# Optimization experiments

Measured on AMD Instinct MI355X. Metric: run time of the kernel, lower is better.

The kernel has to match this reference:

```python
import jax, jax.numpy as jnp
import numpy as np

B, L, D = 16, 8192, 256

def setup_inputs() -> dict:
    key = jax.random.key(0)
    inputs = jax.random.normal(key, (B, L, D), dtype=jnp.float32)
    return {"inputs": inputs}

def reference(inputs) -> jnp.ndarray:
    # position weights: softmax over L of per-token L2 norms
    norms = jnp.linalg.norm(inputs, axis=2)            # [B, L]
    w = jax.nn.softmax(norms, axis=1)                  # [B, L]
    # weighted sum of outer products == X^T diag(w) X, fused as one einsum
    out = jnp.einsum('bl,bld,ble->bde', w, inputs, inputs)  # [B, D, D]
    return out
```

## Files before the change

kernel.cpp:

```cpp
#include <hip/hip_runtime.h>
#include <hip/hip_bf16.h>

#define NB 16
#define NL 8192
#define ND 256
#define KSPLIT 16
#define CHUNK (NL / KSPLIT)
#define BK 64

#define WS_G_OFF 256

typedef __bf16 bf16_t;
typedef __attribute__((ext_vector_type(4))) __bf16 bf16x4;
typedef __attribute__((ext_vector_type(8))) __bf16 bf16x8;
typedef __attribute__((ext_vector_type(4))) float floatx4;

__device__ __forceinline__ int fsw(int col) {
    return ((col >> 2) & 7) ^ ((col & 3) << 1);
}

__global__ __launch_bounds__(1024, 4) void k_gemm(const float* __restrict__ x,
                                                  float* __restrict__ ws,
                                                  float* __restrict__ gram) {
    const int ks = blockIdx.x, b = blockIdx.y;
    const int t = threadIdx.x;
    const int lane = t & 63;
    const int w = __builtin_amdgcn_readfirstlane(t >> 6);
    const int quad = lane >> 4, m = lane & 15;
    const int g = w >> 1, h = w & 1;

    __shared__ bf16_t lds[256 * 64];

    const float* xb = x + (size_t)b * NL * ND;
    const int l0 = ks * CHUNK;

    floatx4 acc[9];
    #pragma unroll
    for (int j = 0; j < 9; ++j)
        #pragma unroll
        for (int r = 0; r < 4; ++r) acc[j][r] = 0.f;

    float e_acc = 0.f;
    float4 xv[4];
    {
        const float* gp = xb + (size_t)(l0 + w * 4) * ND + lane * 4;
        #pragma unroll
        for (int j = 0; j < 4; ++j) xv[j] = *(const float4*)(gp + (size_t)j * ND);
    }

    for (int kk = 0; kk < CHUNK; kk += BK) {
        if (kk) __syncthreads();
        {
            float ss[4];
            #pragma unroll
            for (int j = 0; j < 4; ++j)
                ss[j] = xv[j].x * xv[j].x + xv[j].y * xv[j].y
                      + xv[j].z * xv[j].z + xv[j].w * xv[j].w;
            #pragma unroll
            for (int off = 32; off; off >>= 1) {
                #pragma unroll
                for (int j = 0; j < 4; ++j) ss[j] += __shfl_xor(ss[j], off, 64);
            }
            float s[4];
            #pragma unroll
            for (int j = 0; j < 4; ++j) {
                s[j] = __expf(0.5f * sqrtf(ss[j]));
                e_acc += s[j] * s[j];
            }
            bf16x4 p[4];
            #pragma unroll
            for (int j = 0; j < 4; ++j) {
                const float* vf = (const float*)&xv[j];
                #pragma unroll
                for (int c = 0; c < 4; ++c) p[c][j] = (bf16_t)(vf[c] * s[j]);
            }
            #pragma unroll
            for (int c = 0; c < 4; ++c) {
                const int col = 4 * lane + c;
                *(bf16x4*)(&lds[col * 64 + ((g ^ fsw(col)) << 3) + (h << 2)]) = p[c];
            }
        }
        __syncthreads();
        if (kk + BK < CHUNK) {
            const float* gp = xb + (size_t)(l0 + kk + BK + w * 4) * ND + lane * 4;
            #pragma unroll
            for (int j = 0; j < 4; ++j) xv[j] = *(const float4*)(gp + (size_t)j * ND);
        }
        #pragma unroll
        for (int k2 = 0; k2 < 2; ++k2) {
            const int kcq = k2 * 4 + quad;
            const int col0 = (w << 4) + m;
            const bf16x8 f0 = *(const bf16x8*)(&lds[(col0 << 6) + ((kcq ^ fsw(col0)) << 3)]);
            #pragma unroll
            for (int j = 0; j < 9; ++j) {
                const int col = (((w + j) & 15) << 4) + m;
                const bf16x8 fj = *(const bf16x8*)(&lds[(col << 6) + ((kcq ^ fsw(col)) << 3)]);
                acc[j] = __builtin_amdgcn_mfma_f32_16x16x32_bf16(f0, fj, acc[j], 0, 0, 0);
            }
        }
    }

    __shared__ float red[16];
    if (lane == 0) red[w] = e_acc;
    __syncthreads();
    if (t == 0) {
        float z = 0.f;
        #pragma unroll
        for (int i = 0; i < 16; ++i) z += red[i];
        ws[b * 16 + ks] = z;
    }

    float* gb = gram + (size_t)(ks * NB + b) * 144 * 256;
    #pragma unroll
    for (int j = 0; j < 9; ++j) {
        float* tb = gb + (w * 9 + j) * 256 + quad * 64 + m;
        #pragma unroll
        for (int reg = 0; reg < 4; ++reg) tb[reg * 16] = acc[j][reg];
    }
}

__global__ __launch_bounds__(256) void k_reduce(const float* __restrict__ gram,
                                                const float* __restrict__ ws,
                                                float* __restrict__ out) {
    const int t = threadIdx.x;
    const int sg = t >> 6;
    const int f = t & 63;
    const int gslot = blockIdx.x * 4 + sg;
    const int b = gslot / 144;
    const int slot = gslot - b * 144;
    const int rt = slot / 9;
    const int j = slot - rt * 9;
    const int ct = (rt + j) & 15;
    const int er = f >> 2, ecq = f & 3;

    const float* gp = gram + ((size_t)b * 144 + slot) * 256 + er * 16 + ecq * 4;
    float4 s = make_float4(0.f, 0.f, 0.f, 0.f);
    #pragma unroll
    for (int ks = 0; ks < KSPLIT; ++ks) {
        const float4 v = *(const float4*)(gp + (size_t)ks * (NB * 144 * 256));
        s.x += v.x; s.y += v.y; s.z += v.z; s.w += v.w;
    }

    float z = 0.f;
    #pragma unroll
    for (int ks = 0; ks < KSPLIT; ++ks) z += ws[b * 16 + ks];
    const float zi = 1.0f / z;
    s.x *= zi; s.y *= zi; s.z *= zi; s.w *= zi;

    float* ob = out + (size_t)b * ND * ND;
    *(float4*)(ob + (size_t)(rt * 16 + er) * ND + ct * 16 + ecq * 4) = s;

    __shared__ float lt[4][16][20];
    lt[sg][ecq * 4 + 0][er] = s.x;
    lt[sg][ecq * 4 + 1][er] = s.y;
    lt[sg][ecq * 4 + 2][er] = s.z;
    lt[sg][ecq * 4 + 3][er] = s.w;
    __syncthreads();
    if (j >= 1 && j <= 7) {
        const float4 mv = *(const float4*)&lt[sg][er][ecq * 4];
        *(float4*)(ob + (size_t)(ct * 16 + er) * ND + rt * 16 + ecq * 4) = mv;
    }
}

extern "C" void kernel_launch(void* const* d_in, const int* in_sizes, int n_in,
                              void* d_out, int out_size, void* d_ws, size_t ws_size,
                              hipStream_t stream) {
    const float* x = (const float*)d_in[0];
    float* out = (float*)d_out;
    float* ws = (float*)d_ws;
    float* gram = ws + WS_G_OFF;

    k_gemm<<<dim3(KSPLIT, NB), 1024, 0, stream>>>(x, ws, gram);
    k_reduce<<<dim3(NB * 144 / 4), 256, 0, stream>>>(gram, ws, out);
}
```

Before: 205.8 us.

## Double-buffer LDS tiles and ping-pong register prefetch to drop one barrier per step

```diff
diff --git a/kernel.cpp b/kernel.cpp
--- a/kernel.cpp
+++ b/kernel.cpp
@@ -29,7 +29,7 @@
     const int quad = lane >> 4, m = lane & 15;
     const int g = w >> 1, h = w & 1;
 
-    __shared__ bf16_t lds[256 * 64];
+    __shared__ bf16_t lds[2 * 256 * 64];
 
     const float* xb = x + (size_t)b * NL * ND;
     const int l0 = ks * CHUNK;
@@ -41,63 +41,67 @@
         for (int r = 0; r < 4; ++r) acc[j][r] = 0.f;
 
     float e_acc = 0.f;
-    float4 xv[4];
+    float4 xvA[4], xvB[4];
     {
         const float* gp = xb + (size_t)(l0 + w * 4) * ND + lane * 4;
         #pragma unroll
-        for (int j = 0; j < 4; ++j) xv[j] = *(const float4*)(gp + (size_t)j * ND);
+        for (int j = 0; j < 4; ++j) xvA[j] = *(const float4*)(gp + (size_t)j * ND);
     }
 
-    for (int kk = 0; kk < CHUNK; kk += BK) {
-        if (kk) __syncthreads();
-        {
-            float ss[4];
-            #pragma unroll
-            for (int j = 0; j < 4; ++j)
-                ss[j] = xv[j].x * xv[j].x + xv[j].y * xv[j].y
-                      + xv[j].z * xv[j].z + xv[j].w * xv[j].w;
-            #pragma unroll
-            for (int off = 32; off; off >>= 1) {
-                #pragma unroll
-                for (int j = 0; j < 4; ++j) ss[j] += __shfl_xor(ss[j], off, 64);
-            }
-            float s[4];
-            #pragma unroll
-            for (int j = 0; j < 4; ++j) {
-                s[j] = __expf(0.5f * sqrtf(ss[j]));
-                e_acc += s[j] * s[j];
-            }
-            bf16x4 p[4];
-            #pragma unroll
-            for (int j = 0; j < 4; ++j) {
-                const float* vf = (const float*)&xv[j];
-                #pragma unroll
-                for (int c = 0; c < 4; ++c) p[c][j] = (bf16_t)(vf[c] * s[j]);
-            }
-            #pragma unroll
-            for (int c = 0; c < 4; ++c) {
-                const int col = 4 * lane + c;
-                *(bf16x4*)(&lds[col * 64 + ((g ^ fsw(col)) << 3) + (h << 2)]) = p[c];
-            }
-        }
-        __syncthreads();
+    auto body = [&](float4 (&cur)[4], float4 (&nxt)[4], int kk, int lb) {
         if (kk + BK < CHUNK) {
             const float* gp = xb + (size_t)(l0 + kk + BK + w * 4) * ND + lane * 4;
             #pragma unroll
-            for (int j = 0; j < 4; ++j) xv[j] = *(const float4*)(gp + (size_t)j * ND);
+            for (int j = 0; j < 4; ++j) nxt[j] = *(const float4*)(gp + (size_t)j * ND);
         }
+        float ss[4];
+        #pragma unroll
+        for (int j = 0; j < 4; ++j)
+            ss[j] = cur[j].x * cur[j].x + cur[j].y * cur[j].y
+                  + cur[j].z * cur[j].z + cur[j].w * cur[j].w;
+        #pragma unroll
+        for (int off = 32; off; off >>= 1) {
+            #pragma unroll
+            for (int j = 0; j < 4; ++j) ss[j] += __shfl_xor(ss[j], off, 64);
+        }
+        float s[4];
+        #pragma unroll
+        for (int j = 0; j < 4; ++j) {
+            s[j] = __expf(0.5f * sqrtf(ss[j]));
+            e_acc += s[j] * s[j];
+        }
+        bf16x4 p[4];
+        #pragma unroll
+        for (int j = 0; j < 4; ++j) {
+            const float* vf = (const float*)&cur[j];
+            #pragma unroll
+            for (int c = 0; c < 4; ++c) p[c][j] = (bf16_t)(vf[c] * s[j]);
+        }
+        bf16_t* L = lds + lb * (256 * 64);
+        #pragma unroll
+        for (int c = 0; c < 4; ++c) {
+            const int col = 4 * lane + c;
+            *(bf16x4*)(&L[col * 64 + ((g ^ fsw(col)) << 3) + (h << 2)]) = p[c];
+        }
+        __syncthreads();
         #pragma unroll
         for (int k2 = 0; k2 < 2; ++k2) {
             const int kcq = k2 * 4 + quad;
             const int col0 = (w << 4) + m;
-            const bf16x8 f0 = *(const bf16x8*)(&lds[(col0 << 6) + ((kcq ^ fsw(col0)) << 3)]);
+            const bf16x8 f0 = *(const bf16x8*)(&L[(col0 << 6) + ((kcq ^ fsw(col0)) << 3)]);
             #pragma unroll
             for (int j = 0; j < 9; ++j) {
                 const int col = (((w + j) & 15) << 4) + m;
-                const bf16x8 fj = *(const bf16x8*)(&lds[(col << 6) + ((kcq ^ fsw(col)) << 3)]);
+                const bf16x8 fj = *(const bf16x8*)(&L[(col << 6) + ((kcq ^ fsw(col)) << 3)]);
                 acc[j] = __builtin_amdgcn_mfma_f32_16x16x32_bf16(f0, fj, acc[j], 0, 0, 0);
             }
         }
+    };
+
+    #pragma unroll
+    for (int kk = 0; kk < CHUNK; kk += 2 * BK) {
+        body(xvA, xvB, kk, 0);
+        body(xvB, xvA, kk + BK, 1);
     }
 
     __shared__ float red[16];
```

Measured after the change: 211.8 us. 2.9% more time.

## Use 3x3 tile blocking for symmetric Gram MFMA and DPP wave reduction

Applied to the files above, without the earlier changes.

```diff
diff --git a/kernel.cpp b/kernel.cpp
--- a/kernel.cpp
+++ b/kernel.cpp
@@ -17,6 +17,24 @@
 
 __device__ __forceinline__ int fsw(int col) {
     return ((col >> 2) & 7) ^ ((col & 3) << 1);
+}
+
+__device__ __forceinline__ float wave_sum64(float v) {
+#define DPPADD(ctrl)                                                              \
+    {                                                                             \
+        int s_ = __builtin_amdgcn_update_dpp(0, __builtin_bit_cast(int, v),       \
+                                             ctrl, 0xF, 0xF, true);               \
+        v += __builtin_bit_cast(float, s_);                                       \
+    }
+    DPPADD(0x111)
+    DPPADD(0x112)
+    DPPADD(0x114)
+    DPPADD(0x118)
+    DPPADD(0x142)
+    DPPADD(0x143)
+#undef DPPADD
+    return __builtin_bit_cast(float,
+        __builtin_amdgcn_readlane(__builtin_bit_cast(int, v), 63));
 }
 
 __global__ __launch_bounds__(1024, 4) void k_gemm(const float* __restrict__ x,
@@ -51,20 +69,13 @@
     for (int kk = 0; kk < CHUNK; kk += BK) {
         if (kk) __syncthreads();
         {
-            float ss[4];
-            #pragma unroll
-            for (int j = 0; j < 4; ++j)
-                ss[j] = xv[j].x * xv[j].x + xv[j].y * xv[j].y
-                      + xv[j].z * xv[j].z + xv[j].w * xv[j].w;
-            #pragma unroll
-            for (int off = 32; off; off >>= 1) {
-                #pragma unroll
-                for (int j = 0; j < 4; ++j) ss[j] += __shfl_xor(ss[j], off, 64);
-            }
             float s[4];
             #pragma unroll
             for (int j = 0; j < 4; ++j) {
-                s[j] = __expf(0.5f * sqrtf(ss[j]));
+                float ssl = xv[j].x * xv[j].x + xv[j].y * xv[j].y
+                          + xv[j].z * xv[j].z + xv[j].w * xv[j].w;
+                const float tot = wave_sum64(ssl);
+                s[j] = __expf(0.5f * sqrtf(tot));
                 e_acc += s[j] * s[j];
             }
             bf16x4 p[4];
@@ -89,14 +100,20 @@
         #pragma unroll
         for (int k2 = 0; k2 < 2; ++k2) {
             const int kcq = k2 * 4 + quad;
-            const int col0 = (w << 4) + m;
-            const bf16x8 f0 = *(const bf16x8*)(&lds[(col0 << 6) + ((kcq ^ fsw(col0)) << 3)]);
+            bf16x8 fA[3], fB[3];
             #pragma unroll
-            for (int j = 0; j < 9; ++j) {
-                const int col = (((w + j) & 15) << 4) + m;
-                const bf16x8 fj = *(const bf16x8*)(&lds[(col << 6) + ((kcq ^ fsw(col)) << 3)]);
-                acc[j] = __builtin_amdgcn_mfma_f32_16x16x32_bf16(f0, fj, acc[j], 0, 0, 0);
+            for (int i = 0; i < 3; ++i) {
+                const int colA = (((w + i) & 15) << 4) + m;
+                fA[i] = *(const bf16x8*)(&lds[(colA << 6) + ((kcq ^ fsw(colA)) << 3)]);
+                const int colB = (((w + 2 + 3 * i) & 15) << 4) + m;
+                fB[i] = *(const bf16x8*)(&lds[(colB << 6) + ((kcq ^ fsw(colB)) << 3)]);
             }
+            #pragma unroll
+            for (int i = 0; i < 3; ++i)
+                #pragma unroll
+                for (int j = 0; j < 3; ++j)
+                    acc[i * 3 + j] = __builtin_amdgcn_mfma_f32_16x16x32_bf16(
+                        fA[i], fB[j], acc[i * 3 + j], 0, 0, 0);
         }
     }
 
@@ -128,9 +145,12 @@
     const int gslot = blockIdx.x * 4 + sg;
     const int b = gslot / 144;
     const int slot = gslot - b * 144;
-    const int rt = slot / 9;
-    const int j = slot - rt * 9;
-    const int ct = (rt + j) & 15;
+    const int wv = slot / 9;
+    const int r = slot - wv * 9;
+    const int i = r / 3, jj = r - i * 3;
+    const int rt = (wv + i) & 15;
+    const int d = 2 + 3 * jj - i;
+    const int ct = (rt + d) & 15;
     const int er = f >> 2, ecq = f & 3;
 
     const float* gp = gram + ((size_t)b * 144 + slot) * 256 + er * 16 + ecq * 4;
@@ -156,7 +176,7 @@
     lt[sg][ecq * 4 + 2][er] = s.z;
     lt[sg][ecq * 4 + 3][er] = s.w;
     __syncthreads();
-    if (j >= 1 && j <= 7) {
+    if (d >= 1 && d <= 7) {
         const float4 mv = *(const float4*)&lt[sg][er][ecq * 4];
         *(float4*)(ob + (size_t)(ct * 16 + er) * ND + rt * 16 + ecq * 4) = mv;
     }
```

Measured after the change: 205.2 us. About the same (-0.3%).
